# Kernel tuning notes

Hardware: AMD Instinct MI355X
Metric: run time of the kernel (lower is better)

## Reference

```python
import jax, jax.numpy as jnp
import numpy as np
import math

N, LQ, DIM = 4, 1000, 256
HEADS, DHEAD, DEPTH = 8, 32, 2
LVLS, NPTS, MLP = 5, 4, 512
SCALE = DHEAD ** -0.5
SHAPES = np.array([[128, 128], [64, 64], [32, 32], [16, 16], [8, 8]], np.int32)
AREAS = SHAPES[:, 0] * SHAPES[:, 1]
STARTS = np.concatenate([[0], np.cumsum(AREAS)[:-1]]).astype(np.int32)
LIN = int(AREAS.sum())


def _ln(x, g, b):
    m = jnp.mean(x, -1, keepdims=True)
    v = jnp.var(x, -1, keepdims=True)
    return (x - m) * jax.lax.rsqrt(v + 1e-5) * g + b


def _gelu(x):  # tanh-approx GELU exactly as the torch module
    c = math.sqrt(2.0 / math.pi)
    return 0.5 * x * (1.0 + jnp.tanh(c * (x + 0.044715 * x ** 3)))


def _ms_deform(value, shapes, starts, loc, aw):
    # value [N,Lin,H,D]; loc [N,Lq,H,L,P,2] normalized to [0,1]; aw [N,Lq,H,L,P]
    n, lq, h, L, p, _ = loc.shape
    d = value.shape[-1]
    ni = jnp.arange(n)[:, None, None, None]
    hi = jnp.arange(h)[None, None, :, None]
    out = jnp.zeros((n, lq, h, d), value.dtype)
    for l in range(L):  # fixed small pyramid depth
        Hl, Wl = int(shapes[l, 0]), int(shapes[l, 1])
        s = int(starts[l])
        v = value[:, s:s + Hl * Wl].reshape(n, Hl, Wl, h, d)
        gx = loc[:, :, :, l, :, 0] * Wl - 0.5  # [N,Lq,H,P]
        gy = loc[:, :, :, l, :, 1] * Hl - 0.5
        x0 = jnp.floor(gx); y0 = jnp.floor(gy)
        lx = gx - x0; ly = gy - y0
        x0i = x0.astype(jnp.int32); y0i = y0.astype(jnp.int32)
        def corner(yi, xi):
            ok = ((yi >= 0) & (yi < Hl) & (xi >= 0) & (xi < Wl)).astype(value.dtype)
            g = v[ni, jnp.clip(yi, 0, Hl - 1), jnp.clip(xi, 0, Wl - 1), hi]  # [N,Lq,H,P,D]
            return g * ok[..., None]
        samp = (corner(y0i, x0i) * ((1 - ly) * (1 - lx))[..., None]
                + corner(y0i, x0i + 1) * ((1 - ly) * lx)[..., None]
                + corner(y0i + 1, x0i) * (ly * (1 - lx))[..., None]
                + corner(y0i + 1, x0i + 1) * (ly * lx)[..., None])
        out = out + jnp.einsum('nqhp,nqhpd->nqhd', aw[:, :, :, l], samp)
    return out.reshape(n, lq, h * d)


def _forward(x, src, center_pos, pos_w, pos_b, ln1_g, ln1_b, qkv_w, out_w, out_b,
             ln2_g, ln2_b, off_w, off_b, aw_w, aw_b, val_w, val_b, op_w, op_b,
             ln3_g, ln3_b, ff_w1, ff_b1, ff_w2, ff_b2, spatial_shapes, level_start_index):
    shapes = np.asarray(spatial_shapes)
    starts = np.asarray(level_start_index)
    n, lq, dim = x.shape
    pe = center_pos @ pos_w + pos_b                                   # pos_embedding(center_pos)
    ref = jnp.broadcast_to(center_pos[:, :, None, :], (n, lq, LVLS, 2))
    onorm = jnp.asarray(np.stack([shapes[:, 1], shapes[:, 0]], -1), x.dtype)  # [L,2] = (W,H)
    for i in range(DEPTH):
        # --- self-attention: PreNorm(x + pe) ---
        xn = _ln(x + pe, ln1_g[i], ln1_b[i])
        qkv = xn @ qkv_w[i]
        q, k, v = jnp.split(qkv, 3, axis=-1)
        q = q.reshape(n, lq, HEADS, DHEAD).transpose(0, 2, 1, 3)
        k = k.reshape(n, lq, HEADS, DHEAD).transpose(0, 2, 1, 3)
        v = v.reshape(n, lq, HEADS, DHEAD).transpose(0, 2, 1, 3)
        att = jax.nn.softmax(jnp.einsum('nhid,nhjd->nhij', q, k) * SCALE, axis=-1)
        o = jnp.einsum('nhij,nhjd->nhid', att, v).transpose(0, 2, 1, 3).reshape(n, lq, HEADS * DHEAD)
        x = x + o @ out_w[i] + out_b[i]
        # --- deformable cross-attention: PreNorm_CA norms query and src with same LN ---
        xn = _ln(x, ln2_g[i], ln2_b[i])
        srcn = _ln(src, ln2_g[i], ln2_b[i])
        query = xn + pe
        value = (srcn @ val_w[i] + val_b[i]).reshape(n, -1, HEADS, DHEAD)
        off = (query @ off_w[i] + off_b[i]).reshape(n, lq, HEADS, LVLS, NPTS, 2)
        aw = jax.nn.softmax((query @ aw_w[i] + aw_b[i]).reshape(n, lq, HEADS, LVLS * NPTS), axis=-1)
        aw = aw.reshape(n, lq, HEADS, LVLS, NPTS)
        loc = ref[:, :, None, :, None, :] + off / onorm[None, None, None, :, None, :]
        o = _ms_deform(value, shapes, starts, loc, aw)
        x = x + o @ op_w[i] + op_b[i]
        # --- feedforward: PreNorm ---
        xn = _ln(x, ln3_g[i], ln3_b[i])
        x = x + _gelu(xn @ ff_w1[i] + ff_b1[i]) @ ff_w2[i] + ff_b2[i]
    return x


def setup_inputs() -> dict:
    key = jax.random.key(0)
    ks = iter(jax.random.split(key, 64))
    r = lambda sh, s=0.02: jax.random.normal(next(ks), sh, jnp.float32) * s
    # sampling_offsets bias grid init (as in MSDeformAttn._reset_parameters)
    thetas = np.arange(HEADS) * (2.0 * math.pi / HEADS)
    grid = np.stack([np.cos(thetas), np.sin(thetas)], -1)
    grid = grid / np.abs(grid).max(-1, keepdims=True)
    grid = np.tile(grid[:, None, None, :], (1, LVLS, NPTS, 1)) * (np.arange(NPTS) + 1)[None, None, :, None]
    off_b = jnp.tile(jnp.asarray(grid.reshape(-1), jnp.float32)[None], (DEPTH, 1))
    return dict(
        x=jax.random.normal(next(ks), (N, LQ, DIM), jnp.float32),
        src=jax.random.normal(next(ks), (N, LIN, DIM), jnp.float32),
        center_pos=jax.random.uniform(next(ks), (N, LQ, 2), jnp.float32),
        spatial_shapes=jnp.asarray(SHAPES),
        level_start_index=jnp.asarray(STARTS),
        pos_w=r((2, DIM), 0.5), pos_b=jnp.zeros((DIM,), jnp.float32),
        ln1_g=jnp.ones((DEPTH, DIM), jnp.float32), ln1_b=jnp.zeros((DEPTH, DIM), jnp.float32),
        qkv_w=r((DEPTH, DIM, 3 * HEADS * DHEAD)),
        out_w=r((DEPTH, HEADS * DHEAD, DIM)), out_b=jnp.zeros((DEPTH, DIM), jnp.float32),
        ln2_g=jnp.ones((DEPTH, DIM), jnp.float32), ln2_b=jnp.zeros((DEPTH, DIM), jnp.float32),
        off_w=r((DEPTH, DIM, HEADS * LVLS * NPTS * 2)), off_b=off_b,
        aw_w=r((DEPTH, DIM, HEADS * LVLS * NPTS)), aw_b=jnp.zeros((DEPTH, HEADS * LVLS * NPTS), jnp.float32),
        val_w=r((DEPTH, DIM, HEADS * DHEAD)), val_b=jnp.zeros((DEPTH, HEADS * DHEAD), jnp.float32),
        op_w=r((DEPTH, HEADS * DHEAD, DIM)), op_b=jnp.zeros((DEPTH, DIM), jnp.float32),
        ln3_g=jnp.ones((DEPTH, DIM), jnp.float32), ln3_b=jnp.zeros((DEPTH, DIM), jnp.float32),
        ff_w1=r((DEPTH, DIM, MLP)), ff_b1=jnp.zeros((DEPTH, MLP), jnp.float32),
        ff_w2=r((DEPTH, MLP, DIM)), ff_b2=jnp.zeros((DEPTH, DIM), jnp.float32),
    )


def reference(x, src, center_pos, spatial_shapes, level_start_index, pos_w, pos_b,
              ln1_g, ln1_b, qkv_w, out_w, out_b, ln2_g, ln2_b, off_w, off_b,
              aw_w, aw_b, val_w, val_b, op_w, op_b, ln3_g, ln3_b,
              ff_w1, ff_b1, ff_w2, ff_b2):
    return _forward(x, src, center_pos, pos_w, pos_b, ln1_g, ln1_b, qkv_w, out_w, out_b,
                    ln2_g, ln2_b, off_w, off_b, aw_w, aw_b, val_w, val_b, op_w, op_b,
                    ln3_g, ln3_b, ff_w1, ff_b1, ff_w2, ff_b2, spatial_shapes, level_start_index)
```

## Files before the change

### kernel.cpp

```cpp
#include <hip/hip_runtime.h>
#include <hip/hip_bf16.h>
#include <math.h>

#define DIM 256
#define NB 4
#define LQ 1000
#define MLPD 512
#define LIN 21824
#define ROWS_X 4000
#define ROWS_SRC 87296
#define ATT_SCALE 0.17677669529663687f
#define LDK 72
#define VLAYER ((size_t)ROWS_SRC*256)

typedef __hip_bfloat16 bf16;
typedef __attribute__((ext_vector_type(8))) short short8;
typedef __attribute__((ext_vector_type(4))) float floatx4;

__device__ __forceinline__ float rdv(const void* p, int f, size_t i){
    if (f) return ((const float*)p)[i];
    unsigned u = ((unsigned)((const unsigned short*)p)[i]) << 16;
    union { unsigned u; float f; } c; c.u = u; return c.f;
}
__device__ __forceinline__ short f2bs(float v){
    bf16 h = __float2bfloat16(v);
    return *reinterpret_cast<short*>(&h);
}
__device__ __forceinline__ float bs2f(short s){
    union { unsigned u; float f; } c; c.u = ((unsigned)(unsigned short)s) << 16; return c.f;
}

__global__ void detect_kernel(const void* __restrict__ x, int* __restrict__ flag){
    const unsigned short* u = (const unsigned short*)x;
    int t = threadIdx.x;
    bool hit = false;
    #pragma unroll
    for (int k = 0; k < 4; ++k) {
        unsigned short b = u[(t*4 + k)*2];
        union { unsigned u; float f; } c; c.u = ((unsigned)b) << 16;
        if (!(fabsf(c.f) <= 1000.f)) hit = true;
    }
    unsigned long long m = __ballot(hit);
    __shared__ unsigned long long red[4];
    if ((t & 63) == 0) red[t >> 6] = m;
    __syncthreads();
    if (t == 0) flag[0] = ((red[0]|red[1]|red[2]|red[3]) != 0ULL) ? 1 : 0;
}

struct PrepTab { const void* src[15]; float* dst[17]; int n[17]; int bs[18]; };
__global__ void prep_kernel(PrepTab t, const void* __restrict__ offb,
                            const void* __restrict__ awb, const void* __restrict__ pw,
                            const void* __restrict__ pb, const void* __restrict__ cp,
                            const int* __restrict__ flag){
    int f = flag[0];
    int bid = blockIdx.x;
    int j = 0;
    #pragma unroll 1
    while (bid >= t.bs[j+1]) ++j;
    int i = (bid - t.bs[j])*256 + threadIdx.x;
    if (i >= t.n[j]) return;
    if (j < 15) {
        t.dst[j][i] = t.src[j] ? rdv(t.src[j], f, i) : 0.f;
    } else if (j == 15) {
        int layer = i / 480, idx = i - layer*480;
        float v = (idx < 320) ? rdv(offb, f, (size_t)layer*320 + idx)
                              : rdv(awb,  f, (size_t)layer*160 + idx - 320);
        t.dst[15][i] = v;
    } else {
        int row = i >> 8, c = i & 255;
        float cx = rdv(cp, f, (size_t)row*2), cy = rdv(cp, f, (size_t)row*2 + 1);
        t.dst[16][i] = cx*rdv(pw, f, c) + cy*rdv(pw, f, DIM + c) + rdv(pb, f, c);
    }
}

struct WT { const void* src[8]; short* dst[8]; const float* scl[8];
            int K[8]; int N[8]; int ld[8]; int ro[8]; };
__global__ void wtransall_kernel(WT t, const int* __restrict__ flag){
    int j = blockIdx.z >> 1, b = blockIdx.z & 1;
    int K = t.K[j], N = t.N[j];
    int k0 = blockIdx.x*32, n0 = blockIdx.y*32;
    if (k0 >= K || n0 >= N) return;
    int f = flag[0];
    __shared__ float tt[32][33];
    int tx = threadIdx.x & 31, ty = threadIdx.x >> 5;
    size_t base = (size_t)b * K * N;
    for (int i = ty; i < 32; i += 8) {
        int k = k0 + i, n = n0 + tx;
        tt[i][tx] = (k < K && n < N) ? rdv(t.src[j], f, base + (size_t)k*N + n) : 0.f;
    }
    __syncthreads();
    int ld = t.ld[j], ro = t.ro[j];
    const float* sc = t.scl[j];
    for (int i = ty; i < 32; i += 8) {
        int n = n0 + i, k = k0 + tx;
        if (n < N && k < K) {
            float v = tt[tx][i];
            if (sc) v *= sc[(size_t)b*K + k];
            t.dst[j][(size_t)b*ld*K + (size_t)(ro+n)*K + k] = f2bs(v);
        }
    }
}

struct BFT { const void* W[3]; const float* bv[3]; const float* base[3];
             float* dst[3]; int N[3]; };
__global__ __launch_bounds__(256) void biasfold_kernel(BFT t, const int* __restrict__ flag){
    int f = flag[0];
    int x = blockIdx.x, b = blockIdx.y;
    int j, n;
    if (x < 768)       { j = 0; n = x; }
    else if (x < 1280) { j = 1; n = x - 768; }
    else               { j = 2; n = x - 1280; }
    int N = t.N[j];
    int k = threadIdx.x;
    float part = t.bv[j][(size_t)b*256 + k] *
                 rdv(t.W[j], f, (size_t)b*256*N + (size_t)k*N + n);
    #pragma unroll
    for (int o = 32; o; o >>= 1) part += __shfl_xor(part, o, 64);
    __shared__ float red[4];
    int wave = k >> 6, lane = k & 63;
    if (lane == 0) red[wave] = part;
    __syncthreads();
    if (k == 0) {
        float s = red[0] + red[1] + red[2] + red[3];
        if (t.base[j]) s += t.base[j][(size_t)b*N + n];
        t.dst[j][(size_t)b*N + n] = s;
    }
}

__global__ __launch_bounds__(256) void statsconvx_kernel(const void* __restrict__ src,
        const void* __restrict__ x, const float* __restrict__ pe,
        const int* __restrict__ flag, bf16* __restrict__ srcn,
        float* __restrict__ xf, float2* __restrict__ st){
    int f = flag[0];
    int wave = threadIdx.x >> 6, lane = threadIdx.x & 63;
    int bid = blockIdx.x;
    if (bid < ROWS_SRC/4) {
        int row = bid*4 + wave;
        float v0, v1, v2, v3;
        if (f) {
            float4 xx = *(const float4*)((const float*)src + (size_t)row*DIM + lane*4);
            v0 = xx.x; v1 = xx.y; v2 = xx.z; v3 = xx.w;
        } else {
            ushort4 u = *(const ushort4*)((const unsigned short*)src + (size_t)row*DIM + lane*4);
            v0 = bs2f((short)u.x); v1 = bs2f((short)u.y);
            v2 = bs2f((short)u.z); v3 = bs2f((short)u.w);
        }
        float s  = v0 + v1 + v2 + v3;
        float s2 = v0*v0 + v1*v1 + v2*v2 + v3*v3;
        #pragma unroll
        for (int o = 32; o; o >>= 1) {
            s  += __shfl_xor(s,  o, 64);
            s2 += __shfl_xor(s2, o, 64);
        }
        float mean = s * (1.f/DIM);
        float rstd = rsqrtf(s2 * (1.f/DIM) - mean*mean + 1e-5f);
        ushort4 o4;
        o4.x = (unsigned short)f2bs((v0-mean)*rstd);
        o4.y = (unsigned short)f2bs((v1-mean)*rstd);
        o4.z = (unsigned short)f2bs((v2-mean)*rstd);
        o4.w = (unsigned short)f2bs((v3-mean)*rstd);
        *(ushort4*)((unsigned short*)srcn + (size_t)row*DIM + lane*4) = o4;
    } else {
        int row = (bid - ROWS_SRC/4)*4 + wave;
        float4 v;
        if (f) v = *(const float4*)((const float*)x + (size_t)row*DIM + lane*4);
        else {
            ushort4 u = *(const ushort4*)((const unsigned short*)x + (size_t)row*DIM + lane*4);
            v = make_float4(bs2f((short)u.x), bs2f((short)u.y), bs2f((short)u.z), bs2f((short)u.w));
        }
        *(float4*)(xf + (size_t)row*DIM + lane*4) = v;
        float4 p = *(const float4*)(pe + (size_t)row*DIM + lane*4);
        float a0 = v.x+p.x, a1 = v.y+p.y, a2 = v.z+p.z, a3 = v.w+p.w;
        float s  = a0+a1+a2+a3;
        float s2 = a0*a0+a1*a1+a2*a2+a3*a3;
        #pragma unroll
        for (int o = 32; o; o >>= 1) {
            s  += __shfl_xor(s,  o, 64);
            s2 += __shfl_xor(s2, o, 64);
        }
        if (lane == 0) st[row] = make_float2(s, s2);
    }
}

template<int AMODE>
__global__ __launch_bounds__(256) void mgemm_kernel(
    const void* __restrict__ Asrc, const float2* __restrict__ asums,
    const float* __restrict__ ag, const float* __restrict__ ab,
    const float* __restrict__ Apre, const float* __restrict__ Apost,
    const short* __restrict__ Wt, const float* __restrict__ bias, const float* res,
    void* Cout, int M, int K, int N, int act, int cbf,
    float2* __restrict__ statacc, const float* __restrict__ sepe,
    void* __restrict__ fin, const int* __restrict__ flag){
    __shared__ short As[64*LDK];
    __shared__ short Bs[64*LDK];
    __shared__ float gsh[256], bsh[256];
    int tid = threadIdx.x;
    int wave = tid >> 6, lane = tid & 63;
    int wm = wave >> 1, wn = wave & 1;
    int quad = lane >> 4, l16 = lane & 15;
    int row0 = blockIdx.x*64, col0 = blockIdx.y*64;
    floatx4 acc[2][2];
    #pragma unroll
    for (int i = 0; i < 2; ++i)
        #pragma unroll
        for (int j = 0; j < 2; ++j)
            acc[i][j] = (floatx4){0.f,0.f,0.f,0.f};

    int r  = tid >> 2;
    int kc = (tid & 3) * 16;
    int gr = row0 + r;
    int gc = col0 + r;
    const short8 z8 = {0,0,0,0,0,0,0,0};

    if (AMODE == 3) {
        if (tid < 256) { gsh[tid] = ag[tid]; bsh[tid] = ab[tid]; }
        __syncthreads();
    }
    const float* aux = Apre ? Apre : Apost;
    float mean = 0.f, rstd = 0.f;
    if (AMODE != 2 && gr < M) {
        float2 stt = asums[gr];
        mean = stt.x * (1.f/256.f);
        rstd = rsqrtf(stt.y*(1.f/256.f) - mean*mean + 1e-5f);
    }
    short8 ra0, ra1, rb0, rb1;
    float4 rx0, rx1, rx2, rx3, rq0, rq1, rq2, rq3;
    if (gr < M) {
        if (AMODE == 2) {
            const short8* p = (const short8*)((const short*)Asrc + (size_t)gr*K + kc);
            ra0 = p[0]; ra1 = p[1];
        } else {
            const float4* p = (const float4*)((const float*)Asrc + (size_t)gr*K + kc);
            rx0 = p[0]; rx1 = p[1]; rx2 = p[2]; rx3 = p[3];
            if (aux) {
                const float4* q = (const float4*)(aux + (size_t)gr*K + kc);
                rq0 = q[0]; rq1 = q[1]; rq2 = q[2]; rq3 = q[3];
            }
        }
    }
    if (gc < N) {
        const short8* p = (const short8*)(Wt + (size_t)gc*K + kc);
        rb0 = p[0]; rb1 = p[1];
    }

    for (int k0 = 0; k0 < K; k0 += 64) {
        short8 a0 = z8, a1 = z8;
        if (gr < M) {
            if (AMODE == 2) { a0 = ra0; a1 = ra1; }
            else {
                float av[16] = {rx0.x,rx0.y,rx0.z,rx0.w, rx1.x,rx1.y,rx1.z,rx1.w,
                                rx2.x,rx2.y,rx2.z,rx2.w, rx3.x,rx3.y,rx3.z,rx3.w};
                float qv[16] = {rq0.x,rq0.y,rq0.z,rq0.w, rq1.x,rq1.y,rq1.z,rq1.w,
                                rq2.x,rq2.y,rq2.z,rq2.w, rq3.x,rq3.y,rq3.z,rq3.w};
                if (AMODE == 4) {
                    if (Apre) {
                        #pragma unroll
                        for (int j = 0; j < 16; ++j) av[j] += qv[j];
                    }
                    #pragma unroll
                    for (int j = 0; j < 16; ++j) av[j] = (av[j] - mean)*rstd;
                } else {
                    #pragma unroll
                    for (int j = 0; j < 16; ++j)
                        av[j] = (av[j] - mean)*rstd*gsh[k0+kc+j] + bsh[k0+kc+j];
                    if (Apost) {
                        #pragma unroll
                        for (int j = 0; j < 16; ++j) av[j] += qv[j];
                    }
                }
                #pragma unroll
                for (int j = 0; j < 8; ++j) { a0[j] = f2bs(av[j]); a1[j] = f2bs(av[8+j]); }
            }
        }
        *(short8*)&As[r*LDK + kc]     = a0;
        *(short8*)&As[r*LDK + kc + 8] = a1;
        short8 b0 = z8, b1 = z8;
        if (gc < N) { b0 = rb0; b1 = rb1; }
        *(short8*)&Bs[r*LDK + kc]     = b0;
        *(short8*)&Bs[r*LDK + kc + 8] = b1;
        int kn = k0 + 64;
        if (kn < K) {
            if (gr < M) {
                if (AMODE == 2) {
                    const short8* p = (const short8*)((const short*)Asrc + (size_t)gr*K + kn + kc);
                    ra0 = p[0]; ra1 = p[1];
                } else {
                    const float4* p = (const float4*)((const float*)Asrc + (size_t)gr*K + kn + kc);
                    rx0 = p[0]; rx1 = p[1]; rx2 = p[2]; rx3 = p[3];
                    if (aux) {
                        const float4* q = (const float4*)(aux + (size_t)gr*K + kn + kc);
                        rq0 = q[0]; rq1 = q[1]; rq2 = q[2]; rq3 = q[3];
                    }
                }
            }
            if (gc < N) {
                const short8* p = (const short8*)(Wt + (size_t)gc*K + kn + kc);
                rb0 = p[0]; rb1 = p[1];
            }
        }
        __syncthreads();
        #pragma unroll
        for (int kb = 0; kb < 64; kb += 32) {
            short8 af[2], bfr[2];
            #pragma unroll
            for (int mi = 0; mi < 2; ++mi)
                af[mi] = *(const short8*)&As[(wm*32 + mi*16 + l16)*LDK + kb + quad*8];
            #pragma unroll
            for (int ni = 0; ni < 2; ++ni)
                bfr[ni] = *(const short8*)&Bs[(wn*32 + ni*16 + l16)*LDK + kb + quad*8];
            #pragma unroll
            for (int mi = 0; mi < 2; ++mi)
                #pragma unroll
                for (int ni = 0; ni < 2; ++ni)
                    acc[mi][ni] = __builtin_amdgcn_mfma_f32_16x16x32_bf16(
                        af[mi], bfr[ni], acc[mi][ni], 0, 0, 0);
        }
        __syncthreads();
    }
    float vout[2][2][4];
    #pragma unroll
    for (int mi = 0; mi < 2; ++mi) {
        int rbase = row0 + wm*32 + mi*16 + quad*4;
        #pragma unroll
        for (int ni = 0; ni < 2; ++ni) {
            int c = col0 + wn*32 + ni*16 + l16;
            #pragma unroll
            for (int r2 = 0; r2 < 4; ++r2) {
                int rr = rbase + r2;
                float v = 0.f;
                if (c < N && rr < M) {
                    v = acc[mi][ni][r2];
                    if (bias) v += bias[c];
                    if (act) {
                        float z = fminf(1.5957691216057308f*(v + 0.044715f*v*v*v), 60.f);
                        float e = __expf(z);
                        v = v * e / (e + 1.f);
                    }
                    if (res) v += res[(size_t)rr*N + c];
                }
                vout[mi][ni][r2] = v;
            }
        }
    }
    int fflag = 0;
    if (fin) fflag = flag[0];
    #pragma unroll
    for (int mi = 0; mi < 2; ++mi) {
        int rbase = row0 + wm*32 + mi*16 + quad*4;
        #pragma unroll
        for (int ni = 0; ni < 2; ++ni) {
            int c = col0 + wn*32 + ni*16 + l16;
            if (c >= N) continue;
            #pragma unroll
            for (int r2 = 0; r2 < 4; ++r2) {
                int rr = rbase + r2;
                if (rr >= M) continue;
                float v = vout[mi][ni][r2];
                if (fin) {
                    float w = isfinite(v) ? v : 0.f;
                    if (fflag) ((float*)fin)[(size_t)rr*N + c] = w;
                    else       ((bf16*)fin)[(size_t)rr*N + c] = __float2bfloat16(w);
                } else if (cbf) ((bf16*)Cout)[(size_t)rr*N + c] = __float2bfloat16(v);
                else            ((float*)Cout)[(size_t)rr*N + c] = v;
            }
        }
    }
    if (statacc) {
        #pragma unroll
        for (int mi = 0; mi < 2; ++mi) {
            int rbase = row0 + wm*32 + mi*16 + quad*4;
            #pragma unroll
            for (int r2 = 0; r2 < 4; ++r2) {
                int rr = rbase + r2;
                float sv = 0.f, sq = 0.f;
                #pragma unroll
                for (int ni = 0; ni < 2; ++ni) {
                    int c = col0 + wn*32 + ni*16 + l16;
                    float v = vout[mi][ni][r2];
                    if (sepe && rr < M) v += sepe[(size_t)rr*256 + c];
                    sv += v; sq += v*v;
                }
                #pragma unroll
                for (int o = 1; o < 16; o <<= 1) {
                    sv += __shfl_xor(sv, o, 64);
                    sq += __shfl_xor(sq, o, 64);
                }
                if (l16 == 0 && rr < M) {
                    atomicAdd(&statacc[rr].x, sv);
                    atomicAdd(&statacc[rr].y, sq);
                }
            }
        }
    }
}

__global__ __launch_bounds__(256) void mgemm128_kernel(
    const short* __restrict__ A, const short* __restrict__ Wt,
    const float* __restrict__ bias, bf16* __restrict__ valall){
    const int K = 256;
    __shared__ short As[128*LDK];
    __shared__ short Bs[128*LDK];
    int tid = threadIdx.x;
    int wave = tid >> 6, lane = tid & 63;
    int wm = wave >> 1, wn = wave & 1;
    int quad = lane >> 4, l16 = lane & 15;
    int row0 = blockIdx.x*128, col0 = blockIdx.y*128;
    floatx4 acc[4][4];
    #pragma unroll
    for (int i = 0; i < 4; ++i)
        #pragma unroll
        for (int j = 0; j < 4; ++j)
            acc[i][j] = (floatx4){0.f,0.f,0.f,0.f};

    short8 pa[2][2], pb2[2][2];
    #pragma unroll
    for (int i = 0; i < 2; ++i) {
        int idx = tid + i*256;
        int rr = idx >> 2, kk = (idx & 3)*16;
        const short8* p = (const short8*)(A + (size_t)(row0+rr)*K + kk);
        pa[i][0] = p[0]; pa[i][1] = p[1];
        const short8* pb = (const short8*)(Wt + (size_t)(col0+rr)*K + kk);
        pb2[i][0] = pb[0]; pb2[i][1] = pb[1];
    }
    for (int k0 = 0; k0 < K; k0 += 64) {
        #pragma unroll
        for (int i = 0; i < 2; ++i) {
            int idx = tid + i*256;
            int rr = idx >> 2, kk = (idx & 3)*16;
            *(short8*)&As[rr*LDK + kk]     = pa[i][0];
            *(short8*)&As[rr*LDK + kk + 8] = pa[i][1];
            *(short8*)&Bs[rr*LDK + kk]     = pb2[i][0];
            *(short8*)&Bs[rr*LDK + kk + 8] = pb2[i][1];
        }
        int kn = k0 + 64;
        if (kn < K) {
            #pragma unroll
            for (int i = 0; i < 2; ++i) {
                int idx = tid + i*256;
                int rr = idx >> 2, kk = (idx & 3)*16;
                const short8* p = (const short8*)(A + (size_t)(row0+rr)*K + kn + kk);
                pa[i][0] = p[0]; pa[i][1] = p[1];
                const short8* pb = (const short8*)(Wt + (size_t)(col0+rr)*K + kn + kk);
                pb2[i][0] = pb[0]; pb2[i][1] = pb[1];
            }
        }
        __syncthreads();
        #pragma unroll
        for (int kb = 0; kb < 64; kb += 32) {
            short8 af[4], bfr[4];
            #pragma unroll
            for (int mi = 0; mi < 4; ++mi)
                af[mi] = *(const short8*)&As[(wm*64 + mi*16 + l16)*LDK + kb + quad*8];
            #pragma unroll
            for (int ni = 0; ni < 4; ++ni)
                bfr[ni] = *(const short8*)&Bs[(wn*64 + ni*16 + l16)*LDK + kb + quad*8];
            #pragma unroll
            for (int mi = 0; mi < 4; ++mi)
                #pragma unroll
                for (int ni = 0; ni < 4; ++ni)
                    acc[mi][ni] = __builtin_amdgcn_mfma_f32_16x16x32_bf16(
                        af[mi], bfr[ni], acc[mi][ni], 0, 0, 0);
        }
        __syncthreads();
    }
    #pragma unroll
    for (int mi = 0; mi < 4; ++mi) {
        int rbase = row0 + wm*64 + mi*16 + quad*4;
        #pragma unroll
        for (int ni = 0; ni < 4; ++ni) {
            int c = col0 + wn*64 + ni*16 + l16;
            int l = c >> 8, hc = c & 255;
            int h = hc >> 5, d = hc & 31;
            float bv = bias[c];
            #pragma unroll
            for (int r2 = 0; r2 < 4; ++r2) {
                int rr = rbase + r2;
                unsigned n = (unsigned)rr / (unsigned)LIN;
                int pos = rr - (int)n*LIN;
                valall[(size_t)l*VLAYER + ((size_t)(n*8+h)*LIN + pos)*32 + d] =
                    __float2bfloat16(acc[mi][ni][r2] + bv);
            }
        }
    }
}

__global__ __launch_bounds__(256) void fattn_kernel(const short* __restrict__ qkv,
                                                    bf16* __restrict__ out){
    int nh = blockIdx.y;
    int n = nh >> 3, h = nh & 7;
    int q0 = blockIdx.x * 64;
    __shared__ short Ks[64*40];
    __shared__ short VsT[32*72];
    __shared__ short Ps[64*72];
    int tid = threadIdx.x;
    int wave = tid >> 6, lane = tid & 63;
    int quad = lane >> 4, l16 = lane & 15;
    int r = tid >> 2, c8 = (tid & 3) * 8;
    const short8 z8 = {0,0,0,0,0,0,0,0};

    short8 qf = z8;
    {
        int gq = q0 + wave*16 + l16;
        if (gq < LQ) {
            short8 s = *(const short8*)(qkv + ((size_t)(n*LQ+gq))*768 + h*32 + quad*8);
            #pragma unroll
            for (int j = 0; j < 8; ++j) qf[j] = f2bs(bs2f(s[j]) * ATT_SCALE);
        }
    }
    floatx4 acc[2];
    acc[0] = (floatx4){0.f,0.f,0.f,0.f};
    acc[1] = (floatx4){0.f,0.f,0.f,0.f};
    float m[4], lsum[4];
    #pragma unroll
    for (int i = 0; i < 4; ++i) { m[i] = -3.0e38f; lsum[i] = 0.f; }

    short8 kvp = z8, vvp = z8;
    if (r < LQ) {
        const short* rp = qkv + ((size_t)(n*LQ+r))*768;
        kvp = *(const short8*)(rp + 256 + h*32 + c8);
        vvp = *(const short8*)(rp + 512 + h*32 + c8);
    }
    for (int k0 = 0; k0 < LQ; k0 += 64) {
        *(short8*)&Ks[r*40 + c8] = kvp;
        #pragma unroll
        for (int j = 0; j < 8; ++j) VsT[(c8+j)*72 + r] = vvp[j];
        short8 kvn = z8, vvn = z8;
        if (k0 + 64 < LQ) {
            int gk = k0 + 64 + r;
            if (gk < LQ) {
                const short* rp = qkv + ((size_t)(n*LQ+gk))*768;
                kvn = *(const short8*)(rp + 256 + h*32 + c8);
                vvn = *(const short8*)(rp + 512 + h*32 + c8);
            }
        }
        __syncthreads();
        floatx4 s4[4];
        #pragma unroll
        for (int kg = 0; kg < 4; ++kg) {
            short8 bfr = *(const short8*)&Ks[(kg*16 + l16)*40 + quad*8];
            s4[kg] = __builtin_amdgcn_mfma_f32_16x16x32_bf16(
                qf, bfr, (floatx4){0.f,0.f,0.f,0.f}, 0, 0, 0);
        }
        if (k0 + 64 > LQ) {
            #pragma unroll
            for (int kg = 0; kg < 4; ++kg)
                if (k0 + kg*16 + l16 >= LQ)
                    s4[kg] = (floatx4){-3.0e38f,-3.0e38f,-3.0e38f,-3.0e38f};
        }
        float fac[4], psum[4];
        #pragma unroll
        for (int r2 = 0; r2 < 4; ++r2) {
            float v = fmaxf(fmaxf(s4[0][r2], s4[1][r2]), fmaxf(s4[2][r2], s4[3][r2]));
            v = fmaxf(v, __shfl_xor(v, 1, 64));
            v = fmaxf(v, __shfl_xor(v, 2, 64));
            v = fmaxf(v, __shfl_xor(v, 4, 64));
            v = fmaxf(v, __shfl_xor(v, 8, 64));
            float mn = fmaxf(m[r2], v);
            fac[r2] = __expf(m[r2] - mn);
            m[r2] = mn;
            psum[r2] = 0.f;
        }
        #pragma unroll
        for (int kg = 0; kg < 4; ++kg)
            #pragma unroll
            for (int r2 = 0; r2 < 4; ++r2) {
                float pv = __expf(s4[kg][r2] - m[r2]);
                psum[r2] += pv;
                Ps[(wave*16 + quad*4 + r2)*72 + kg*16 + l16] = f2bs(pv);
            }
        #pragma unroll
        for (int r2 = 0; r2 < 4; ++r2) {
            psum[r2] += __shfl_xor(psum[r2], 1, 64);
            psum[r2] += __shfl_xor(psum[r2], 2, 64);
            psum[r2] += __shfl_xor(psum[r2], 4, 64);
            psum[r2] += __shfl_xor(psum[r2], 8, 64);
            lsum[r2] = lsum[r2]*fac[r2] + psum[r2];
        }
        #pragma unroll
        for (int ni = 0; ni < 2; ++ni)
            #pragma unroll
            for (int r2 = 0; r2 < 4; ++r2)
                acc[ni][r2] *= fac[r2];
        #pragma unroll
        for (int kb = 0; kb < 64; kb += 32) {
            short8 pf = *(const short8*)&Ps[(wave*16 + l16)*72 + kb + quad*8];
            #pragma unroll
            for (int ni = 0; ni < 2; ++ni) {
                short8 vf = *(const short8*)&VsT[(ni*16 + l16)*72 + kb + quad*8];
                acc[ni] = __builtin_amdgcn_mfma_f32_16x16x32_bf16(pf, vf, acc[ni], 0, 0, 0);
            }
        }
        __syncthreads();
        kvp = kvn; vvp = vvn;
    }
    #pragma unroll
    for (int r2 = 0; r2 < 4; ++r2) {
        int row = q0 + wave*16 + quad*4 + r2;
        if (row >= LQ) continue;
        float inv = 1.f / lsum[r2];
        #pragma unroll
        for (int ni = 0; ni < 2; ++ni)
            out[((size_t)(n*LQ+row))*256 + h*32 + ni*16 + l16] =
                __float2bfloat16(acc[ni][r2] * inv);
    }
}

__global__ __launch_bounds__(256) void sample2_kernel(
        const bf16* __restrict__ value, const float* __restrict__ offaw,
        const float* __restrict__ cp, bf16* __restrict__ out){
    int nq = blockIdx.x;
    int n = nq / LQ;
    int d = threadIdx.x & 31, h = threadIdx.x >> 5;
    float cx = cp[nq*2], cy = cp[nq*2+1];
    const float* rowp = offaw + (size_t)nq*480;
    float o0 = rowp[h*40 + d];
    float o1 = (d < 8) ? rowp[h*40 + 32 + d] : 0.f;
    float logit = (d < 20) ? rowp[320 + h*20 + d] : -3.0e38f;
    float mx = logit;
    #pragma unroll
    for (int off = 16; off; off >>= 1) mx = fmaxf(mx, __shfl_xor(mx, off, 32));
    float p = (d < 20) ? __expf(logit - mx) : 0.f;
    float sm = p;
    #pragma unroll
    for (int off = 16; off; off >>= 1) sm += __shfl_xor(sm, off, 32);
    p *= (1.f / sm);

    const int HW[5] = {128,64,32,16,8};
    const int ST[5] = {0,16384,20480,21504,21760};
    float acc = 0.f;
    #pragma unroll
    for (int l = 0; l < 5; ++l) {
        int hw = HW[l];
        float fhw = (float)hw;
        size_t vb = ((size_t)(n*8 + h)*LIN + ST[l])*32 + d;
        #pragma unroll
        for (int pi = 0; pi < 4; ++pi) {
            const int idx = l*4 + pi;
            float w  = __shfl(p, idx, 32);
            float ox = (2*idx < 32)   ? __shfl(o0, 2*idx, 32)   : __shfl(o1, 2*idx-32, 32);
            float oy = (2*idx+1 < 32) ? __shfl(o0, 2*idx+1, 32) : __shfl(o1, 2*idx+1-32, 32);
            float gx = cx*fhw + ox - 0.5f;
            float gy = cy*fhw + oy - 0.5f;
            float x0f = floorf(gx), y0f = floorf(gy);
            float lx = gx - x0f, ly = gy - y0f;
            int x0 = (int)x0f, y0 = (int)y0f;
            int x1 = x0 + 1, y1 = y0 + 1;
            bool bx0 = (unsigned)x0 < (unsigned)hw, bx1 = (unsigned)x1 < (unsigned)hw;
            bool by0 = (unsigned)y0 < (unsigned)hw, by1 = (unsigned)y1 < (unsigned)hw;
            int x0c = min(max(x0, 0), hw-1), x1c = min(max(x1, 0), hw-1);
            int y0c = min(max(y0, 0), hw-1), y1c = min(max(y1, 0), hw-1);
            float v00 = __bfloat162float(value[vb + (size_t)(y0c*hw + x0c)*32]);
            float v01 = __bfloat162float(value[vb + (size_t)(y0c*hw + x1c)*32]);
            float v10 = __bfloat162float(value[vb + (size_t)(y1c*hw + x0c)*32]);
            float v11 = __bfloat162float(value[vb + (size_t)(y1c*hw + x1c)*32]);
            float w00 = (bx0 && by0) ? (1.f-ly)*(1.f-lx)*w : 0.f;
            float w01 = (bx1 && by0) ? (1.f-ly)*lx*w       : 0.f;
            float w10 = (bx0 && by1) ? ly*(1.f-lx)*w       : 0.f;
            float w11 = (bx1 && by1) ? ly*lx*w             : 0.f;
            acc = fmaf(w00, v00, acc);
            acc = fmaf(w01, v01, acc);
            acc = fmaf(w10, v10, acc);
            acc = fmaf(w11, v11, acc);
        }
    }
    out[(size_t)nq*256 + h*32 + d] = __float2bfloat16(acc);
}

extern "C" void kernel_launch(void* const* d_in, const int* in_sizes, int n_in,
                              void* d_out, int out_size, void* d_ws, size_t ws_size,
                              hipStream_t stream){
    const void* x_raw  = d_in[0];
    const void* src    = d_in[1];
    const void* cp_raw = d_in[2];
    char* ws = (char*)d_ws;
    size_t off = 0;
    auto alloc = [&](size_t bytes){ size_t p = off; off += (bytes + 255) & ~(size_t)255; return p; };
    int*   flag  = (int*)(ws + alloc(256));
    float* xf    = (float*)(ws + alloc((size_t)ROWS_X*DIM*4));
    float* pe    = (float*)(ws + alloc((size_t)ROWS_X*DIM*4));
    bf16*  tmpb  = (bf16*)(ws + alloc((size_t)ROWS_X*DIM*2));
    bf16*  qkv   = (bf16*)(ws + alloc((size_t)ROWS_X*768*2));
    bf16*  ffh   = (bf16*)(ws + alloc((size_t)ROWS_X*MLPD*2));
    float* offaw = (float*)(ws + alloc((size_t)ROWS_X*480*4));
    float* cpf   = (float*)(ws + alloc((size_t)ROWS_X*2*4));
    float* oab   = (float*)(ws + alloc((size_t)2*480*4));
    float2* statbuf = (float2*)(ws + alloc((size_t)6*ROWS_X*8));
    float* qkvB  = (float*)(ws + alloc((size_t)2*768*4));
    float* ff1B  = (float*)(ws + alloc((size_t)2*512*4));
    float* valB  = (float*)(ws + alloc((size_t)2*256*4));
    const int sidx[13] = {5,6,7,8,11,12,13,19,21,22,23,25,27};
    const int ssz[13]  = {512,256,512,512,512,512,512,512,512,512,512,1024,512};
    float* sp[13];
    for (int j = 0; j < 13; ++j) sp[j] = (float*)(ws + alloc((size_t)ssz[j]*4));
    short* qkvT = (short*)(ws + alloc((size_t)2*768*256*2));
    short* outT = (short*)(ws + alloc((size_t)2*256*256*2));
    short* oawT = (short*)(ws + alloc((size_t)2*480*256*2));
    short* valT = (short*)(ws + alloc((size_t)2*256*256*2));
    short* opT  = (short*)(ws + alloc((size_t)2*256*256*2));
    short* ff1T = (short*)(ws + alloc((size_t)2*512*256*2));
    short* ff2T = (short*)(ws + alloc((size_t)2*256*512*2));
    bf16*  srcn = (bf16*)(ws + alloc((size_t)ROWS_SRC*DIM*2));
    bf16*  valall = (bf16*)(ws + alloc((size_t)2*ROWS_SRC*DIM*2));
    (void)ws_size; (void)in_sizes; (void)n_in; (void)out_size;

    float* ln1_g = sp[2];  float* ln1_b = sp[3];
    float* out_b = sp[4];
    float* ln2_g = sp[5];  float* ln2_b = sp[6];
    float* val_b = sp[7];  float* op_b  = sp[8];
    float* ln3_g = sp[9];  float* ln3_b = sp[10];
    float* ff_b1 = sp[11]; float* ff_b2 = sp[12];

    detect_kernel<<<1, 256, 0, stream>>>(x_raw, flag);
    {
        PrepTab pt;
        int nb = 0;
        int nn[17];
        for (int j = 0; j < 13; ++j) { pt.src[j] = d_in[sidx[j]]; pt.dst[j] = sp[j]; nn[j] = ssz[j]; }
        pt.src[13] = cp_raw;  pt.dst[13] = cpf;  nn[13] = ROWS_X*2;
        pt.src[14] = nullptr; pt.dst[14] = (float*)(statbuf + ROWS_X); nn[14] = 5*ROWS_X*2;
        pt.dst[15] = oab;  nn[15] = 960;
        pt.dst[16] = pe;   nn[16] = ROWS_X*DIM;
        for (int j = 0; j < 17; ++j) {
            pt.n[j] = nn[j];
            pt.bs[j] = nb;
            nb += (nn[j] + 255)/256;
        }
        pt.bs[17] = nb;
        prep_kernel<<<nb, 256, 0, stream>>>(pt, d_in[15], d_in[17], d_in[5], d_in[6],
                                            cp_raw, flag);
    }
    statsconvx_kernel<<<ROWS_SRC/4 + ROWS_X/4, 256, 0, stream>>>(
        src, x_raw, pe, flag, srcn, xf, statbuf);
    {
        WT wt;
        const int widx[8] = {9,10,14,16,18,20,24,26};
        short* wdst[8] = {qkvT, outT, oawT, oawT, valT, opT, ff1T, ff2T};
        const float* wscl[8] = {ln1_g, nullptr, nullptr, nullptr, ln2_g, nullptr, ln3_g, nullptr};
        const int wK[8]  = {256,256,256,256,256,256,256,512};
        const int wN[8]  = {768,256,320,160,256,256,512,256};
        const int wld[8] = {768,256,480,480,256,256,512,256};
        const int wro[8] = {0,0,0,320,0,0,0,0};
        for (int j = 0; j < 8; ++j) {
            wt.src[j] = d_in[widx[j]]; wt.dst[j] = wdst[j]; wt.scl[j] = wscl[j];
            wt.K[j] = wK[j]; wt.N[j] = wN[j]; wt.ld[j] = wld[j]; wt.ro[j] = wro[j];
        }
        wtransall_kernel<<<dim3(16,24,16), 256, 0, stream>>>(wt, flag);
    }
    {
        BFT bt;
        bt.W[0] = d_in[9];  bt.bv[0] = ln1_b; bt.base[0] = nullptr; bt.dst[0] = qkvB; bt.N[0] = 768;
        bt.W[1] = d_in[24]; bt.bv[1] = ln3_b; bt.base[1] = ff_b1;   bt.dst[1] = ff1B; bt.N[1] = 512;
        bt.W[2] = d_in[18]; bt.bv[2] = ln2_b; bt.base[2] = val_b;   bt.dst[2] = valB; bt.N[2] = 256;
        biasfold_kernel<<<dim3(1536,2), 256, 0, stream>>>(bt, flag);
    }
    mgemm128_kernel<<<dim3(ROWS_SRC/128, 4), 256, 0, stream>>>(
        (const short*)srcn, valT, valB, valall);

    int gmx = (ROWS_X + 63) / 64;
    for (int i = 0; i < 2; ++i) {
        float2* stA = statbuf + (size_t)(i ? 3 : 0)*ROWS_X;
        float2* stO = statbuf + (size_t)(i ? 4 : 1)*ROWS_X;
        float2* stF = statbuf + (size_t)(i ? 5 : 2)*ROWS_X;
        mgemm_kernel<4><<<dim3(gmx,12), 256, 0, stream>>>(
            xf, stA, nullptr, nullptr, pe, nullptr,
            qkvT + (size_t)i*768*256, qkvB + i*768, nullptr, qkv,
            ROWS_X, 256, 768, 0, 1, nullptr, nullptr, nullptr, flag);
        fattn_kernel<<<dim3(16,32), 256, 0, stream>>>((const short*)qkv, tmpb);
        mgemm_kernel<2><<<dim3(gmx,4), 256, 0, stream>>>(
            tmpb, nullptr, nullptr, nullptr, nullptr, nullptr,
            outT + (size_t)i*256*256, out_b + i*DIM, xf, xf,
            ROWS_X, 256, 256, 0, 0, stO, nullptr, nullptr, flag);
        mgemm_kernel<3><<<dim3(gmx,8), 256, 0, stream>>>(
            xf, stO, ln2_g + i*DIM, ln2_b + i*DIM, nullptr, pe,
            oawT + (size_t)i*480*256, oab + i*480, nullptr, offaw,
            ROWS_X, 256, 480, 0, 0, nullptr, nullptr, nullptr, flag);
        sample2_kernel<<<ROWS_X, 256, 0, stream>>>(
            valall + (size_t)i*VLAYER, offaw, cpf, tmpb);
        mgemm_kernel<2><<<dim3(gmx,4), 256, 0, stream>>>(
            tmpb, nullptr, nullptr, nullptr, nullptr, nullptr,
            opT + (size_t)i*256*256, op_b + i*DIM, xf, xf,
            ROWS_X, 256, 256, 0, 0, stF, nullptr, nullptr, flag);
        mgemm_kernel<4><<<dim3(gmx,8), 256, 0, stream>>>(
            xf, stF, nullptr, nullptr, nullptr, nullptr,
            ff1T + (size_t)i*512*256, ff1B + i*MLPD, nullptr, ffh,
            ROWS_X, 256, 512, 1, 1, nullptr, nullptr, nullptr, flag);
        if (i == 0) {
            mgemm_kernel<2><<<dim3(gmx,4), 256, 0, stream>>>(
                ffh, nullptr, nullptr, nullptr, nullptr, nullptr,
                ff2T + (size_t)i*256*512, ff_b2 + i*DIM, xf, xf,
                ROWS_X, 512, 256, 0, 0, statbuf + (size_t)3*ROWS_X, pe, nullptr, flag);
        } else {
            mgemm_kernel<2><<<dim3(gmx,4), 256, 0, stream>>>(
                ffh, nullptr, nullptr, nullptr, nullptr, nullptr,
                ff2T + (size_t)i*256*512, ff_b2 + i*DIM, xf, xf,
                ROWS_X, 512, 256, 0, 0, nullptr, nullptr, d_out, flag);
        }
    }
}
```

Baseline: 591.4 us.

## Widen GEMM column tile to 128 and stage value-projection output through LDS

The small-row GEMM now covers 128 output columns per block instead of 64, so each A tile (including its fused LayerNorm conversion) is reused across twice as many columns, and the grid shrinks to match. The value-projection GEMM writes its bf16 results into shared memory first and then emits contiguous 16-byte stores into the head-major value layout, replacing scattered 2-byte stores. Its grid is also transposed so the four column blocks of one row block run next to each other, which may improve reuse of the A rows in cache. The costs are more accumulator registers and LDS per block, and fewer blocks for the 4000-row GEMMs, which may lower occupancy and parallelism.

```diff
diff --git a/kernel.cpp b/kernel.cpp
--- a/kernel.cpp
+++ b/kernel.cpp
@@ -192,28 +192,29 @@
     float2* __restrict__ statacc, const float* __restrict__ sepe,
     void* __restrict__ fin, const int* __restrict__ flag){
     __shared__ short As[64*LDK];
-    __shared__ short Bs[64*LDK];
+    __shared__ short Bs[128*LDK];
     __shared__ float gsh[256], bsh[256];
     int tid = threadIdx.x;
     int wave = tid >> 6, lane = tid & 63;
     int wm = wave >> 1, wn = wave & 1;
     int quad = lane >> 4, l16 = lane & 15;
-    int row0 = blockIdx.x*64, col0 = blockIdx.y*64;
-    floatx4 acc[2][2];
+    int row0 = blockIdx.x*64, col0 = blockIdx.y*128;
+    floatx4 acc[2][4];
     #pragma unroll
     for (int i = 0; i < 2; ++i)
         #pragma unroll
-        for (int j = 0; j < 2; ++j)
+        for (int j = 0; j < 4; ++j)
             acc[i][j] = (floatx4){0.f,0.f,0.f,0.f};
 
     int r  = tid >> 2;
     int kc = (tid & 3) * 16;
     int gr = row0 + r;
-    int gc = col0 + r;
+    int gc0 = col0 + r;
+    int gc1 = col0 + 64 + r;
     const short8 z8 = {0,0,0,0,0,0,0,0};
 
     if (AMODE == 3) {
-        if (tid < 256) { gsh[tid] = ag[tid]; bsh[tid] = ab[tid]; }
+        gsh[tid] = ag[tid]; bsh[tid] = ab[tid];
         __syncthreads();
     }
     const float* aux = Apre ? Apre : Apost;
@@ -223,7 +224,7 @@
         mean = stt.x * (1.f/256.f);
         rstd = rsqrtf(stt.y*(1.f/256.f) - mean*mean + 1e-5f);
     }
-    short8 ra0, ra1, rb0, rb1;
+    short8 ra0, ra1, rb0, rb1, rb2, rb3;
     float4 rx0, rx1, rx2, rx3, rq0, rq1, rq2, rq3;
     if (gr < M) {
         if (AMODE == 2) {
@@ -238,9 +239,13 @@
             }
         }
     }
-    if (gc < N) {
-        const short8* p = (const short8*)(Wt + (size_t)gc*K + kc);
+    if (gc0 < N) {
+        const short8* p = (const short8*)(Wt + (size_t)gc0*K + kc);
         rb0 = p[0]; rb1 = p[1];
+    }
+    if (gc1 < N) {
+        const short8* p = (const short8*)(Wt + (size_t)gc1*K + kc);
+        rb2 = p[0]; rb3 = p[1];
     }
 
     for (int k0 = 0; k0 < K; k0 += 64) {
@@ -274,10 +279,13 @@
         }
         *(short8*)&As[r*LDK + kc]     = a0;
         *(short8*)&As[r*LDK + kc + 8] = a1;
-        short8 b0 = z8, b1 = z8;
-        if (gc < N) { b0 = rb0; b1 = rb1; }
-        *(short8*)&Bs[r*LDK + kc]     = b0;
-        *(short8*)&Bs[r*LDK + kc + 8] = b1;
+        short8 b0 = z8, b1 = z8, b2 = z8, b3 = z8;
+        if (gc0 < N) { b0 = rb0; b1 = rb1; }
+        if (gc1 < N) { b2 = rb2; b3 = rb3; }
+        *(short8*)&Bs[r*LDK + kc]          = b0;
+        *(short8*)&Bs[r*LDK + kc + 8]      = b1;
+        *(short8*)&Bs[(64+r)*LDK + kc]     = b2;
+        *(short8*)&Bs[(64+r)*LDK + kc + 8] = b3;
         int kn = k0 + 64;
         if (kn < K) {
             if (gr < M) {
@@ -293,37 +301,41 @@
                     }
                 }
             }
-            if (gc < N) {
-                const short8* p = (const short8*)(Wt + (size_t)gc*K + kn + kc);
+            if (gc0 < N) {
+                const short8* p = (const short8*)(Wt + (size_t)gc0*K + kn + kc);
                 rb0 = p[0]; rb1 = p[1];
             }
+            if (gc1 < N) {
+                const short8* p = (const short8*)(Wt + (size_t)gc1*K + kn + kc);
+                rb2 = p[0]; rb3 = p[1];
+            }
         }
         __syncthreads();
         #pragma unroll
         for (int kb = 0; kb < 64; kb += 32) {
-            short8 af[2], bfr[2];
+            short8 af[2], bfr[4];
             #pragma unroll
             for (int mi = 0; mi < 2; ++mi)
                 af[mi] = *(const short8*)&As[(wm*32 + mi*16 + l16)*LDK + kb + quad*8];
             #pragma unroll
-            for (int ni = 0; ni < 2; ++ni)
-                bfr[ni] = *(const short8*)&Bs[(wn*32 + ni*16 + l16)*LDK + kb + quad*8];
+            for (int ni = 0; ni < 4; ++ni)
+                bfr[ni] = *(const short8*)&Bs[(wn*64 + ni*16 + l16)*LDK + kb + quad*8];
             #pragma unroll
             for (int mi = 0; mi < 2; ++mi)
                 #pragma unroll
-                for (int ni = 0; ni < 2; ++ni)
+                for (int ni = 0; ni < 4; ++ni)
                     acc[mi][ni] = __builtin_amdgcn_mfma_f32_16x16x32_bf16(
                         af[mi], bfr[ni], acc[mi][ni], 0, 0, 0);
         }
         __syncthreads();
     }
-    float vout[2][2][4];
+    float vout[2][4][4];
     #pragma unroll
     for (int mi = 0; mi < 2; ++mi) {
         int rbase = row0 + wm*32 + mi*16 + quad*4;
         #pragma unroll
-        for (int ni = 0; ni < 2; ++ni) {
-            int c = col0 + wn*32 + ni*16 + l16;
+        for (int ni = 0; ni < 4; ++ni) {
+            int c = col0 + wn*64 + ni*16 + l16;
             #pragma unroll
             for (int r2 = 0; r2 < 4; ++r2) {
                 int rr = rbase + r2;
@@ -348,8 +360,8 @@
     for (int mi = 0; mi < 2; ++mi) {
         int rbase = row0 + wm*32 + mi*16 + quad*4;
         #pragma unroll
-        for (int ni = 0; ni < 2; ++ni) {
-            int c = col0 + wn*32 + ni*16 + l16;
+        for (int ni = 0; ni < 4; ++ni) {
+            int c = col0 + wn*64 + ni*16 + l16;
             if (c >= N) continue;
             #pragma unroll
             for (int r2 = 0; r2 < 4; ++r2) {
@@ -374,10 +386,10 @@
                 int rr = rbase + r2;
                 float sv = 0.f, sq = 0.f;
                 #pragma unroll
-                for (int ni = 0; ni < 2; ++ni) {
-                    int c = col0 + wn*32 + ni*16 + l16;
+                for (int ni = 0; ni < 4; ++ni) {
+                    int c = col0 + wn*64 + ni*16 + l16;
                     float v = vout[mi][ni][r2];
-                    if (sepe && rr < M) v += sepe[(size_t)rr*256 + c];
+                    if (sepe && rr < M && c < N) v += sepe[(size_t)rr*256 + c];
                     sv += v; sq += v*v;
                 }
                 #pragma unroll
@@ -398,13 +410,14 @@
     const short* __restrict__ A, const short* __restrict__ Wt,
     const float* __restrict__ bias, bf16* __restrict__ valall){
     const int K = 256;
-    __shared__ short As[128*LDK];
-    __shared__ short Bs[128*LDK];
+    __shared__ short lds[2*128*LDK];
+    short* As = lds;
+    short* Bs = lds + 128*LDK;
     int tid = threadIdx.x;
     int wave = tid >> 6, lane = tid & 63;
     int wm = wave >> 1, wn = wave & 1;
     int quad = lane >> 4, l16 = lane & 15;
-    int row0 = blockIdx.x*128, col0 = blockIdx.y*128;
+    int row0 = blockIdx.y*128, col0 = blockIdx.x*128;
     floatx4 acc[4][4];
     #pragma unroll
     for (int i = 0; i < 4; ++i)
@@ -463,23 +476,35 @@
         }
         __syncthreads();
     }
+    short* Cs = lds;
     #pragma unroll
     for (int mi = 0; mi < 4; ++mi) {
-        int rbase = row0 + wm*64 + mi*16 + quad*4;
+        int lr = wm*64 + mi*16 + quad*4;
         #pragma unroll
         for (int ni = 0; ni < 4; ++ni) {
-            int c = col0 + wn*64 + ni*16 + l16;
-            int l = c >> 8, hc = c & 255;
-            int h = hc >> 5, d = hc & 31;
-            float bv = bias[c];
-            #pragma unroll
-            for (int r2 = 0; r2 < 4; ++r2) {
-                int rr = rbase + r2;
-                unsigned n = (unsigned)rr / (unsigned)LIN;
-                int pos = rr - (int)n*LIN;
-                valall[(size_t)l*VLAYER + ((size_t)(n*8+h)*LIN + pos)*32 + d] =
-                    __float2bfloat16(acc[mi][ni][r2] + bv);
-            }
+            int lc = wn*64 + ni*16 + l16;
+            float bv = bias[col0 + lc];
+            #pragma unroll
+            for (int r2 = 0; r2 < 4; ++r2)
+                Cs[(lr + r2)*136 + lc] = f2bs(acc[mi][ni][r2] + bv);
+        }
+    }
+    __syncthreads();
+    #pragma unroll
+    for (int g = 0; g < 4; ++g) {
+        int cbase = col0 + g*32;
+        int l = cbase >> 8, h = (cbase & 255) >> 5;
+        #pragma unroll
+        for (int p = 0; p < 2; ++p) {
+            int idx = p*256 + tid;
+            int rr2 = idx >> 2;
+            int dc = (idx & 3) * 8;
+            short8 v = *(const short8*)&Cs[rr2*136 + g*32 + dc];
+            int grr = row0 + rr2;
+            unsigned n = (unsigned)grr / (unsigned)LIN;
+            int pos = grr - (int)n*LIN;
+            *(short8*)((short*)valall + (size_t)l*VLAYER
+                       + ((size_t)(n*8+h)*LIN + pos)*32 + dc) = v;
         }
     }
 }
@@ -753,7 +778,7 @@
         bt.W[2] = d_in[18]; bt.bv[2] = ln2_b; bt.base[2] = val_b;   bt.dst[2] = valB; bt.N[2] = 256;
         biasfold_kernel<<<dim3(1536,2), 256, 0, stream>>>(bt, flag);
     }
-    mgemm128_kernel<<<dim3(ROWS_SRC/128, 4), 256, 0, stream>>>(
+    mgemm128_kernel<<<dim3(4, ROWS_SRC/128), 256, 0, stream>>>(
         (const short*)srcn, valT, valB, valall);
 
     int gmx = (ROWS_X + 63) / 64;
@@ -761,36 +786,36 @@
         float2* stA = statbuf + (size_t)(i ? 3 : 0)*ROWS_X;
         float2* stO = statbuf + (size_t)(i ? 4 : 1)*ROWS_X;
         float2* stF = statbuf + (size_t)(i ? 5 : 2)*ROWS_X;
-        mgemm_kernel<4><<<dim3(gmx,12), 256, 0, stream>>>(
+        mgemm_kernel<4><<<dim3(gmx,6), 256, 0, stream>>>(
             xf, stA, nullptr, nullptr, pe, nullptr,
             qkvT + (size_t)i*768*256, qkvB + i*768, nullptr, qkv,
             ROWS_X, 256, 768, 0, 1, nullptr, nullptr, nullptr, flag);
         fattn_kernel<<<dim3(16,32), 256, 0, stream>>>((const short*)qkv, tmpb);
-        mgemm_kernel<2><<<dim3(gmx,4), 256, 0, stream>>>(
+        mgemm_kernel<2><<<dim3(gmx,2), 256, 0, stream>>>(
             tmpb, nullptr, nullptr, nullptr, nullptr, nullptr,
             outT + (size_t)i*256*256, out_b + i*DIM, xf, xf,
             ROWS_X, 256, 256, 0, 0, stO, nullptr, nullptr, flag);
-        mgemm_kernel<3><<<dim3(gmx,8), 256, 0, stream>>>(
+        mgemm_kernel<3><<<dim3(gmx,4), 256, 0, stream>>>(
             xf, stO, ln2_g + i*DIM, ln2_b + i*DIM, nullptr, pe,
             oawT + (size_t)i*480*256, oab + i*480, nullptr, offaw,
             ROWS_X, 256, 480, 0, 0, nullptr, nullptr, nullptr, flag);
         sample2_kernel<<<ROWS_X, 256, 0, stream>>>(
             valall + (size_t)i*VLAYER, offaw, cpf, tmpb);
-        mgemm_kernel<2><<<dim3(gmx,4), 256, 0, stream>>>(
+        mgemm_kernel<2><<<dim3(gmx,2), 256, 0, stream>>>(
             tmpb, nullptr, nullptr, nullptr, nullptr, nullptr,
             opT + (size_t)i*256*256, op_b + i*DIM, xf, xf,
             ROWS_X, 256, 256, 0, 0, stF, nullptr, nullptr, flag);
-        mgemm_kernel<4><<<dim3(gmx,8), 256, 0, stream>>>(
+        mgemm_kernel<4><<<dim3(gmx,4), 256, 0, stream>>>(
             xf, stF, nullptr, nullptr, nullptr, nullptr,
             ff1T + (size_t)i*512*256, ff1B + i*MLPD, nullptr, ffh,
             ROWS_X, 256, 512, 1, 1, nullptr, nullptr, nullptr, flag);
         if (i == 0) {
-            mgemm_kernel<2><<<dim3(gmx,4), 256, 0, stream>>>(
+            mgemm_kernel<2><<<dim3(gmx,2), 256, 0, stream>>>(
                 ffh, nullptr, nullptr, nullptr, nullptr, nullptr,
                 ff2T + (size_t)i*256*512, ff_b2 + i*DIM, xf, xf,
                 ROWS_X, 512, 256, 0, 0, statbuf + (size_t)3*ROWS_X, pe, nullptr, flag);
         } else {
-            mgemm_kernel<2><<<dim3(gmx,4), 256, 0, stream>>>(
+            mgemm_kernel<2><<<dim3(gmx,2), 256, 0, stream>>>(
                 ffh, nullptr, nullptr, nullptr, nullptr, nullptr,
                 ff2T + (size_t)i*256*512, ff_b2 + i*DIM, xf, xf,
                 ROWS_X, 512, 256, 0, 0, nullptr, nullptr, d_out, flag);
```

New measurement: 629.3 us. +6.4%, slower.

## Stage value GEMM epilogue through LDS for vectorized stores and swizzle blocks

Applied to the files above, without the earlier changes.

The value-projection GEMM epilogue now writes results to shared memory first, then emits 16-byte vectorized stores into the head-major value layout instead of scattered 2-byte stores. The grid is flattened and blocks are remapped so groups of 8 row panels share column tiles, aiming for better L2 reuse of weights and A rows. It also drops a redundant tid<256 guard. The extra LDS round trip and barrier add some latency.

```diff
diff --git a/kernel.cpp b/kernel.cpp
--- a/kernel.cpp
+++ b/kernel.cpp
@@ -213,7 +213,7 @@
     const short8 z8 = {0,0,0,0,0,0,0,0};
 
     if (AMODE == 3) {
-        if (tid < 256) { gsh[tid] = ag[tid]; bsh[tid] = ab[tid]; }
+        gsh[tid] = ag[tid]; bsh[tid] = ab[tid];
         __syncthreads();
     }
     const float* aux = Apre ? Apre : Apost;
@@ -398,13 +398,25 @@
     const short* __restrict__ A, const short* __restrict__ Wt,
     const float* __restrict__ bias, bf16* __restrict__ valall){
     const int K = 256;
-    __shared__ short As[128*LDK];
-    __shared__ short Bs[128*LDK];
+    __shared__ short lds[2*128*LDK];
+    short* As = lds;
+    short* Bs = lds + 128*LDK;
     int tid = threadIdx.x;
     int wave = tid >> 6, lane = tid & 63;
     int wm = wave >> 1, wn = wave & 1;
     int quad = lane >> 4, l16 = lane & 15;
-    int row0 = blockIdx.x*128, col0 = blockIdx.y*128;
+    int bid = blockIdx.x;
+    int panel, col;
+    if (bid < 2720) {
+        int g = bid >> 5, w = bid & 31;
+        panel = g*8 + (w & 7);
+        col = w >> 3;
+    } else {
+        int idx = bid - 2720;
+        panel = 680 + (idx >> 2);
+        col = idx & 3;
+    }
+    int row0 = panel*128, col0 = col*128;
     floatx4 acc[4][4];
     #pragma unroll
     for (int i = 0; i < 4; ++i)
@@ -463,23 +475,35 @@
         }
         __syncthreads();
     }
+    short* Cs = lds;
     #pragma unroll
     for (int mi = 0; mi < 4; ++mi) {
-        int rbase = row0 + wm*64 + mi*16 + quad*4;
+        int lr = wm*64 + mi*16 + quad*4;
         #pragma unroll
         for (int ni = 0; ni < 4; ++ni) {
-            int c = col0 + wn*64 + ni*16 + l16;
-            int l = c >> 8, hc = c & 255;
-            int h = hc >> 5, d = hc & 31;
-            float bv = bias[c];
-            #pragma unroll
-            for (int r2 = 0; r2 < 4; ++r2) {
-                int rr = rbase + r2;
-                unsigned n = (unsigned)rr / (unsigned)LIN;
-                int pos = rr - (int)n*LIN;
-                valall[(size_t)l*VLAYER + ((size_t)(n*8+h)*LIN + pos)*32 + d] =
-                    __float2bfloat16(acc[mi][ni][r2] + bv);
-            }
+            int lc = wn*64 + ni*16 + l16;
+            float bv = bias[col0 + lc];
+            #pragma unroll
+            for (int r2 = 0; r2 < 4; ++r2)
+                Cs[(lr + r2)*136 + lc] = f2bs(acc[mi][ni][r2] + bv);
+        }
+    }
+    __syncthreads();
+    #pragma unroll
+    for (int g = 0; g < 4; ++g) {
+        int cbase = col0 + g*32;
+        int l = cbase >> 8, h = (cbase & 255) >> 5;
+        #pragma unroll
+        for (int p = 0; p < 2; ++p) {
+            int idx = p*256 + tid;
+            int rr2 = idx >> 2;
+            int dc = (idx & 3) * 8;
+            short8 v = *(const short8*)&Cs[rr2*136 + g*32 + dc];
+            int grr = row0 + rr2;
+            unsigned n = (unsigned)grr / (unsigned)LIN;
+            int pos = grr - (int)n*LIN;
+            *(short8*)((short*)valall + (size_t)l*VLAYER
+                       + ((size_t)(n*8+h)*LIN + pos)*32 + dc) = v;
         }
     }
 }
@@ -753,7 +777,7 @@
         bt.W[2] = d_in[18]; bt.bv[2] = ln2_b; bt.base[2] = val_b;   bt.dst[2] = valB; bt.N[2] = 256;
         biasfold_kernel<<<dim3(1536,2), 256, 0, stream>>>(bt, flag);
     }
-    mgemm128_kernel<<<dim3(ROWS_SRC/128, 4), 256, 0, stream>>>(
+    mgemm128_kernel<<<(ROWS_SRC/128)*4, 256, 0, stream>>>(
         (const short*)srcn, valT, valB, valall);
 
     int gmx = (ROWS_X + 63) / 64;
```

Measured after the change: 574.3 us. -2.9%, faster.
